# Kernel tuning notes

Hardware: AMD Instinct MI355X
Metric: run time of the kernel (lower is better)

## Reference

```python
import jax, jax.numpy as jnp
import numpy as np

B, C, H, Wd = 16, 256, 64, 64
D_MODEL = 256


def setup_inputs() -> dict:
    key = jax.random.key(0)
    kx, kw = jax.random.split(key)
    x = jax.random.normal(kx, (B, C, H, Wd), dtype=jnp.float32)
    # 1x1 conv weight [out_c=1+2*d_model, in_c], scaled like kaiming-ish init
    W = jax.random.normal(kw, (1 + 2 * D_MODEL, C), dtype=jnp.float32) / np.sqrt(C)
    return {"x": x, "W": W}


def reference(x, W):
    b, c, h, w = x.shape
    d = (W.shape[0] - 1) // 2
    n = h * w
    xf = x.reshape(b, c, n)                      # [b, c, N]
    qkv = jnp.einsum('oc,bcn->bon', W, xf)       # 1x1 conv == channel GEMM
    q = qkv[:, :1]                               # [b, 1, N]
    k = qkv[:, 1:1 + d]                          # [b, d, N]
    v = qkv[:, 1 + d:]                           # [b, d, N]
    scores = jax.nn.softmax(q, axis=-1)          # softmax over tokens
    ctx = jnp.sum(k * scores, axis=-1, keepdims=True)  # [b, d, 1]
    out = jax.nn.relu(v) * ctx                   # gated ReLU(v)
    return out.reshape(b, d, h, w)
```

## Files before the change

kernel.cpp:

```cpp
#include <hip/hip_runtime.h>
#include <cstdint>
#include <cstddef>

#define NB 16
#define NC 256
#define NN 4096
#define ND 256

typedef unsigned short u16;
typedef unsigned int u32;

typedef __attribute__((ext_vector_type(8))) short short8;
typedef __attribute__((ext_vector_type(4))) float f32x4;

__device__ __forceinline__ u16 f2bf(float f) {
  union { float f; u32 u; } v; v.f = f;
  u32 r = v.u + 0x7FFFu + ((v.u >> 16) & 1u);
  return (u16)(r >> 16);
}
__device__ __forceinline__ float bf2f(u16 h) {
  union { u32 u; float f; } v; v.u = ((u32)h) << 16; return v.f;
}

__global__ __launch_bounds__(256) void k_zero(float* __restrict__ q,
                                              float* __restrict__ xs) {
  const int i = blockIdx.x * 256 + threadIdx.x;
  if (i < NB * NN) q[i] = 0.f;
  else xs[i - NB * NN] = 0.f;
}

__global__ __launch_bounds__(256) void k_cast_transpose_q(const float* __restrict__ x,
                                                          const float* __restrict__ W,
                                                          u16* __restrict__ xbT,
                                                          float* __restrict__ q) {
  __shared__ __align__(16) u16 tile[64 * 68];
  __shared__ float qred[16 * 64];
  const int t = threadIdx.x;
  const int b = blockIdx.z, c0 = blockIdx.y * 64, n0 = blockIdx.x * 64;
  const float* xb = x + (size_t)(b * NC + c0) * NN + n0;
  const int nl = (t & 15) * 4;
  float qacc[4] = {0.f, 0.f, 0.f, 0.f};
#pragma unroll
  for (int i = 0; i < 4; ++i) {
    int cl = (t >> 4) + i * 16;
    float4 v = *(const float4*)(xb + (size_t)cl * NN + nl);
    const float wq = W[c0 + cl];
    qacc[0] += wq * v.x; qacc[1] += wq * v.y;
    qacc[2] += wq * v.z; qacc[3] += wq * v.w;
    tile[(nl + 0) * 68 + cl] = f2bf(v.x);
    tile[(nl + 1) * 68 + cl] = f2bf(v.y);
    tile[(nl + 2) * 68 + cl] = f2bf(v.z);
    tile[(nl + 3) * 68 + cl] = f2bf(v.w);
  }
#pragma unroll
  for (int j = 0; j < 4; ++j) qred[(t >> 4) * 64 + nl + j] = qacc[j];
  __syncthreads();
  u16* ob = xbT + (size_t)(b * NN + n0) * NC + c0;
#pragma unroll
  for (int i = 0; i < 4; ++i) {
    int e = t + i * 256;
    int rn = e >> 4;
    int rc = (e & 15) * 4;
    ushort4 pv = *(const ushort4*)&tile[rn * 68 + rc];
    *(ushort4*)(ob + (size_t)rn * NC + rc) = pv;
  }
  if (t < 64) {
    float s = 0.f;
#pragma unroll
    for (int k = 0; k < 16; ++k) s += qred[k * 64 + t];
    atomicAdd(&q[b * NN + n0 + t], s);
  }
}

__global__ __launch_bounds__(256) void k_softmax(const float* __restrict__ q,
                                                 float* __restrict__ s) {
  __shared__ float red[256];
  const int b = blockIdx.x, t = threadIdx.x;
  const float* qb = q + b * NN;
  float v[16];
  float m = -3.4e38f;
#pragma unroll
  for (int i = 0; i < 16; ++i) { v[i] = qb[t + i * 256]; m = fmaxf(m, v[i]); }
  red[t] = m;
  __syncthreads();
  for (int off = 128; off > 0; off >>= 1) {
    if (t < off) red[t] = fmaxf(red[t], red[t + off]);
    __syncthreads();
  }
  const float M = red[0];
  __syncthreads();
  float sum = 0.f;
#pragma unroll
  for (int i = 0; i < 16; ++i) { v[i] = __expf(v[i] - M); sum += v[i]; }
  red[t] = sum;
  __syncthreads();
  for (int off = 128; off > 0; off >>= 1) {
    if (t < off) red[t] += red[t + off];
    __syncthreads();
  }
  const float inv = 1.f / red[0];
  float* sb = s + b * NN;
#pragma unroll
  for (int i = 0; i < 16; ++i) sb[t + i * 256] = v[i] * inv;
}

__global__ __launch_bounds__(256) void k_xs(const u16* __restrict__ xbT,
                                            const float* __restrict__ s,
                                            float* __restrict__ xs) {
  const int t = threadIdx.x;
  const int b = blockIdx.y, n0 = blockIdx.x * 128;
  const u16* xp = xbT + ((size_t)(b * NN + n0)) * NC + t;
  const float* sp = s + b * NN + n0;
  float acc = 0.f;
#pragma unroll 8
  for (int j = 0; j < 128; ++j) {
    acc += bf2f(xp[(size_t)j * NC]) * sp[j];
  }
  atomicAdd(&xs[b * NC + t], acc);
}

__global__ __launch_bounds__(256) void k_ctx(const float* __restrict__ W,
                                             const float* __restrict__ xs,
                                             float* __restrict__ ctx) {
  __shared__ float sx[NC];
  const int b = blockIdx.x, d = threadIdx.x;
  sx[d] = xs[b * NC + d];
  __syncthreads();
  const float* wk = W + (size_t)(1 + d) * NC;
  float acc = 0.f;
#pragma unroll 4
  for (int c = 0; c < NC; ++c) acc += wk[c] * sx[c];
  ctx[b * NC + d] = acc;
}

__global__ __launch_bounds__(256) void k_castwv(const float* __restrict__ W,
                                                u16* __restrict__ wvb) {
  const int i = (blockIdx.x * 256 + threadIdx.x) * 4;
  const float4 v = *(const float4*)(W + (size_t)(1 + ND) * NC + i);
  ushort4 o;
  o.x = f2bf(v.x); o.y = f2bf(v.y); o.z = f2bf(v.z); o.w = f2bf(v.w);
  *(ushort4*)(wvb + i) = o;
}

#define BM 128
#define BN 128
#define BK 64

__global__ __launch_bounds__(256) void k_gemm(const u16* __restrict__ xbT,
                                              const u16* __restrict__ wvb,
                                              const float* __restrict__ ctx,
                                              float* __restrict__ out) {
  __shared__ __align__(16) u16 As[BM * BK];
  __shared__ __align__(16) u16 Bs[BN * BK];
  const int t = threadIdx.x;
  const int b = blockIdx.z;
  const int d0 = blockIdx.y * BM;
  const int n0 = blockIdx.x * BN;
  const int lane = t & 63, w = t >> 6;
  const int wd = (w & 1) * 64, wn = (w >> 1) * 64;
  const int quad = lane >> 4, l15 = lane & 15;

  f32x4 acc[4][4];
#pragma unroll
  for (int mi = 0; mi < 4; ++mi)
#pragma unroll
    for (int ni = 0; ni < 4; ++ni)
      acc[mi][ni] = (f32x4){0.f, 0.f, 0.f, 0.f};

  const int rstg = t >> 3;
  const int l8 = (((t & 7) ^ (rstg & 7))) * 8;
  const u16* gA = wvb + (size_t)(d0 + rstg) * NC + l8;
  const u16* gB = xbT + (size_t)(b * NN + n0 + rstg) * NC + l8;
  const int ldst = 8 * t;

  const int pq0 = ((0 * 4 + quad) ^ (l15 & 7)) * 8;
  const int pq1 = ((1 * 4 + quad) ^ (l15 & 7)) * 8;

  for (int kk = 0; kk < NC; kk += BK) {
    __syncthreads();
#pragma unroll
    for (int i = 0; i < 4; ++i) {
      __builtin_amdgcn_global_load_lds(
          (const __attribute__((address_space(1))) u32*)(gA + kk + (size_t)(32 * i) * NC),
          (__attribute__((address_space(3))) u32*)(As + 2048 * i + ldst), 16, 0, 0);
      __builtin_amdgcn_global_load_lds(
          (const __attribute__((address_space(1))) u32*)(gB + kk + (size_t)(32 * i) * NC),
          (__attribute__((address_space(3))) u32*)(Bs + 2048 * i + ldst), 16, 0, 0);
    }
    __syncthreads();

#pragma unroll
    for (int kq = 0; kq < 2; ++kq) {
      const int pq = kq ? pq1 : pq0;
      short8 af[4], bfr[4];
#pragma unroll
      for (int mi = 0; mi < 4; ++mi)
        af[mi] = *(const short8*)&As[(wd + mi * 16 + l15) * BK + pq];
#pragma unroll
      for (int ni = 0; ni < 4; ++ni)
        bfr[ni] = *(const short8*)&Bs[(wn + ni * 16 + l15) * BK + pq];
#pragma unroll
      for (int mi = 0; mi < 4; ++mi)
#pragma unroll
        for (int ni = 0; ni < 4; ++ni)
          acc[mi][ni] = __builtin_amdgcn_mfma_f32_16x16x32_bf16(af[mi], bfr[ni],
                                                                acc[mi][ni], 0, 0, 0);
    }
  }

#pragma unroll
  for (int mi = 0; mi < 4; ++mi) {
#pragma unroll
    for (int r = 0; r < 4; ++r) {
      const int d = d0 + wd + mi * 16 + quad * 4 + r;
      const float cx = ctx[b * NC + d];
      float* op = out + (size_t)(b * NC + d) * NN + n0 + wn + l15;
#pragma unroll
      for (int ni = 0; ni < 4; ++ni) {
        float v = acc[mi][ni][r];
        op[ni * 16] = fmaxf(v, 0.f) * cx;
      }
    }
  }
}

extern "C" void kernel_launch(void* const* d_in, const int* in_sizes, int n_in,
                              void* d_out, int out_size, void* d_ws, size_t ws_size,
                              hipStream_t stream) {
  const float* x = (const float*)d_in[0];
  const float* W = (const float*)d_in[1];
  float* out = (float*)d_out;

  char* ws = (char*)d_ws;
  u16* xbT   = (u16*)ws;
  float* q   = (float*)(ws + 33554432);
  float* s   = (float*)(ws + 33554432 + 262144);
  float* xs  = (float*)(ws + 33554432 + 524288);
  float* ctx = (float*)(ws + 33554432 + 540672);
  u16* wvb   = (u16*)(ws + 33554432 + 557056);

  k_zero<<<272, 256, 0, stream>>>(q, xs);
  k_cast_transpose_q<<<dim3(64, 4, 16), 256, 0, stream>>>(x, W, xbT, q);
  k_softmax<<<16, 256, 0, stream>>>(q, s);
  k_xs<<<dim3(32, 16), 256, 0, stream>>>(xbT, s, xs);
  k_ctx<<<16, 256, 0, stream>>>(W, xs, ctx);
  k_castwv<<<64, 256, 0, stream>>>(W, wvb);
  k_gemm<<<dim3(32, 2, 16), 256, 0, stream>>>(xbT, wvb, ctx, out);
}
```

Measured before the change: 155.0 us.

## Fuse q projection, online softmax partials and cast into one pass, enlarge GEMM tile

Replaces the zero, cast-transpose, softmax, xs-reduction, ctx and weight-cast kernels with two kernels. The first computes q, per-tile softmax max/sum and weighted x partials over a 64-token tile covering all channels, and also writes the transposed bf16 x. The second combines the partials flash-style and computes ctx while casting Wv. This removes the atomics and the extra re-read of xbT. The GEMM moves to 256x128 tiles with 512 threads covering all of d per block, which halves grid size and increases LDS use.

```diff
diff --git a/kernel.cpp b/kernel.cpp
--- a/kernel.cpp
+++ b/kernel.cpp
@@ -22,142 +22,120 @@
   union { u32 u; float f; } v; v.u = ((u32)h) << 16; return v.f;
 }
 
-__global__ __launch_bounds__(256) void k_zero(float* __restrict__ q,
-                                              float* __restrict__ xs) {
-  const int i = blockIdx.x * 256 + threadIdx.x;
-  if (i < NB * NN) q[i] = 0.f;
-  else xs[i - NB * NN] = 0.f;
-}
-
-__global__ __launch_bounds__(256) void k_cast_transpose_q(const float* __restrict__ x,
-                                                          const float* __restrict__ W,
-                                                          u16* __restrict__ xbT,
-                                                          float* __restrict__ q) {
-  __shared__ __align__(16) u16 tile[64 * 68];
+__global__ __launch_bounds__(256) void k_fuse1(const float* __restrict__ x,
+                                               const float* __restrict__ W,
+                                               u16* __restrict__ xbT,
+                                               float* __restrict__ pm,
+                                               float* __restrict__ pl,
+                                               float* __restrict__ pacc) {
+  __shared__ __align__(16) u16 tile[64 * 264];
   __shared__ float qred[16 * 64];
+  __shared__ float qv[64];
+  __shared__ float pv[64];
   const int t = threadIdx.x;
-  const int b = blockIdx.z, c0 = blockIdx.y * 64, n0 = blockIdx.x * 64;
-  const float* xb = x + (size_t)(b * NC + c0) * NN + n0;
+  const int b = blockIdx.y, n0 = blockIdx.x * 64;
+  const float* xb = x + (size_t)b * NC * NN + n0;
   const int nl = (t & 15) * 4;
-  float qacc[4] = {0.f, 0.f, 0.f, 0.f};
-#pragma unroll
-  for (int i = 0; i < 4; ++i) {
-    int cl = (t >> 4) + i * 16;
-    float4 v = *(const float4*)(xb + (size_t)cl * NN + nl);
-    const float wq = W[c0 + cl];
-    qacc[0] += wq * v.x; qacc[1] += wq * v.y;
-    qacc[2] += wq * v.z; qacc[3] += wq * v.w;
-    tile[(nl + 0) * 68 + cl] = f2bf(v.x);
-    tile[(nl + 1) * 68 + cl] = f2bf(v.y);
-    tile[(nl + 2) * 68 + cl] = f2bf(v.z);
-    tile[(nl + 3) * 68 + cl] = f2bf(v.w);
-  }
-#pragma unroll
-  for (int j = 0; j < 4; ++j) qred[(t >> 4) * 64 + nl + j] = qacc[j];
-  __syncthreads();
-  u16* ob = xbT + (size_t)(b * NN + n0) * NC + c0;
-#pragma unroll
-  for (int i = 0; i < 4; ++i) {
-    int e = t + i * 256;
-    int rn = e >> 4;
-    int rc = (e & 15) * 4;
-    ushort4 pv = *(const ushort4*)&tile[rn * 68 + rc];
-    *(ushort4*)(ob + (size_t)rn * NC + rc) = pv;
-  }
+  const int cg = t >> 4;
+  float q0 = 0.f, q1 = 0.f, q2 = 0.f, q3 = 0.f;
+#pragma unroll
+  for (int i = 0; i < 16; ++i) {
+    const int c = cg + i * 16;
+    float4 v = *(const float4*)(xb + (size_t)c * NN + nl);
+    const float wq = W[c];
+    q0 += wq * v.x; q1 += wq * v.y; q2 += wq * v.z; q3 += wq * v.w;
+    tile[(nl + 0) * 264 + c] = f2bf(v.x);
+    tile[(nl + 1) * 264 + c] = f2bf(v.y);
+    tile[(nl + 2) * 264 + c] = f2bf(v.z);
+    tile[(nl + 3) * 264 + c] = f2bf(v.w);
+  }
+  qred[cg * 64 + nl + 0] = q0;
+  qred[cg * 64 + nl + 1] = q1;
+  qred[cg * 64 + nl + 2] = q2;
+  qred[cg * 64 + nl + 3] = q3;
+  __syncthreads();
   if (t < 64) {
     float s = 0.f;
 #pragma unroll
     for (int k = 0; k < 16; ++k) s += qred[k * 64 + t];
-    atomicAdd(&q[b * NN + n0 + t], s);
-  }
-}
-
-__global__ __launch_bounds__(256) void k_softmax(const float* __restrict__ q,
-                                                 float* __restrict__ s) {
-  __shared__ float red[256];
-  const int b = blockIdx.x, t = threadIdx.x;
-  const float* qb = q + b * NN;
-  float v[16];
-  float m = -3.4e38f;
-#pragma unroll
-  for (int i = 0; i < 16; ++i) { v[i] = qb[t + i * 256]; m = fmaxf(m, v[i]); }
-  red[t] = m;
-  __syncthreads();
-  for (int off = 128; off > 0; off >>= 1) {
-    if (t < off) red[t] = fmaxf(red[t], red[t + off]);
-    __syncthreads();
-  }
-  const float M = red[0];
-  __syncthreads();
-  float sum = 0.f;
-#pragma unroll
-  for (int i = 0; i < 16; ++i) { v[i] = __expf(v[i] - M); sum += v[i]; }
-  red[t] = sum;
-  __syncthreads();
-  for (int off = 128; off > 0; off >>= 1) {
-    if (t < off) red[t] += red[t + off];
-    __syncthreads();
-  }
-  const float inv = 1.f / red[0];
-  float* sb = s + b * NN;
-#pragma unroll
-  for (int i = 0; i < 16; ++i) sb[t + i * 256] = v[i] * inv;
-}
-
-__global__ __launch_bounds__(256) void k_xs(const u16* __restrict__ xbT,
-                                            const float* __restrict__ s,
-                                            float* __restrict__ xs) {
-  const int t = threadIdx.x;
-  const int b = blockIdx.y, n0 = blockIdx.x * 128;
-  const u16* xp = xbT + ((size_t)(b * NN + n0)) * NC + t;
-  const float* sp = s + b * NN + n0;
+    qv[t] = s;
+  }
+  __syncthreads();
+  float m = qv[0];
+#pragma unroll 16
+  for (int n = 1; n < 64; ++n) m = fmaxf(m, qv[n]);
+  if (t < 64) pv[t] = __expf(qv[t] - m);
+  __syncthreads();
   float acc = 0.f;
 #pragma unroll 8
-  for (int j = 0; j < 128; ++j) {
-    acc += bf2f(xp[(size_t)j * NC]) * sp[j];
-  }
-  atomicAdd(&xs[b * NC + t], acc);
-}
-
-__global__ __launch_bounds__(256) void k_ctx(const float* __restrict__ W,
-                                             const float* __restrict__ xs,
-                                             float* __restrict__ ctx) {
+  for (int n = 0; n < 64; ++n) acc += bf2f(tile[n * 264 + t]) * pv[n];
+  pacc[((size_t)b * 64 + blockIdx.x) * NC + t] = acc;
+  if (t == 0) {
+    float l = 0.f;
+    for (int n = 0; n < 64; ++n) l += pv[n];
+    pm[b * 64 + blockIdx.x] = m;
+    pl[b * 64 + blockIdx.x] = l;
+  }
+  u16* ob = xbT + (size_t)(b * NN + n0) * NC;
+#pragma unroll
+  for (int i = 0; i < 8; ++i) {
+    const int e = t + i * 256;
+    const int rn = e >> 5;
+    const int rc = (e & 31) * 8;
+    *(short8*)(ob + (size_t)rn * NC + rc) = *(const short8*)&tile[rn * 264 + rc];
+  }
+}
+
+__global__ __launch_bounds__(256) void k_combine(const float* __restrict__ W,
+                                                 const float* __restrict__ pm,
+                                                 const float* __restrict__ pl,
+                                                 const float* __restrict__ pacc,
+                                                 float* __restrict__ ctx,
+                                                 u16* __restrict__ wvb) {
+  __shared__ float sm[64], sl[64], sw[64];
   __shared__ float sx[NC];
-  const int b = blockIdx.x, d = threadIdx.x;
-  sx[d] = xs[b * NC + d];
-  __syncthreads();
-  const float* wk = W + (size_t)(1 + d) * NC;
-  float acc = 0.f;
+  const int b = blockIdx.x, t = threadIdx.x;
+  if (t < 64) { sm[t] = pm[b * 64 + t]; sl[t] = pl[b * 64 + t]; }
+  __syncthreads();
+  float M = -3.4e38f;
+#pragma unroll 16
+  for (int i = 0; i < 64; ++i) M = fmaxf(M, sm[i]);
+  if (t < 64) sw[t] = __expf(sm[t] - M);
+  __syncthreads();
+  float L = 0.f;
+#pragma unroll 16
+  for (int i = 0; i < 64; ++i) L += sw[i] * sl[i];
+  float xsc = 0.f;
+#pragma unroll 8
+  for (int i = 0; i < 64; ++i) xsc += sw[i] * pacc[((size_t)b * 64 + i) * NC + t];
+  sx[t] = xsc / L;
+  __syncthreads();
+  const float* wk = W + (size_t)(1 + t) * NC;
+  float a = 0.f;
 #pragma unroll 4
-  for (int c = 0; c < NC; ++c) acc += wk[c] * sx[c];
-  ctx[b * NC + d] = acc;
-}
-
-__global__ __launch_bounds__(256) void k_castwv(const float* __restrict__ W,
-                                                u16* __restrict__ wvb) {
-  const int i = (blockIdx.x * 256 + threadIdx.x) * 4;
-  const float4 v = *(const float4*)(W + (size_t)(1 + ND) * NC + i);
-  ushort4 o;
-  o.x = f2bf(v.x); o.y = f2bf(v.y); o.z = f2bf(v.z); o.w = f2bf(v.w);
-  *(ushort4*)(wvb + i) = o;
-}
-
-#define BM 128
+  for (int c = 0; c < NC; ++c) a += wk[c] * sx[c];
+  ctx[b * NC + t] = a;
+  const float* wv = W + (size_t)(1 + ND) * NC + (size_t)b * 16 * NC;
+  u16* wo = wvb + (size_t)b * 16 * NC;
+#pragma unroll
+  for (int i = 0; i < 16; ++i) wo[i * NC + t] = f2bf(wv[i * NC + t]);
+}
+
+#define BM 256
 #define BN 128
 #define BK 64
 
-__global__ __launch_bounds__(256) void k_gemm(const u16* __restrict__ xbT,
+__global__ __launch_bounds__(512) void k_gemm(const u16* __restrict__ xbT,
                                               const u16* __restrict__ wvb,
                                               const float* __restrict__ ctx,
                                               float* __restrict__ out) {
   __shared__ __align__(16) u16 As[BM * BK];
   __shared__ __align__(16) u16 Bs[BN * BK];
   const int t = threadIdx.x;
-  const int b = blockIdx.z;
-  const int d0 = blockIdx.y * BM;
+  const int b = blockIdx.y;
   const int n0 = blockIdx.x * BN;
   const int lane = t & 63, w = t >> 6;
-  const int wd = (w & 1) * 64, wn = (w >> 1) * 64;
+  const int wd = (w >> 1) * 64, wn = (w & 1) * 64;
   const int quad = lane >> 4, l15 = lane & 15;
 
   f32x4 acc[4][4];
@@ -168,8 +146,8 @@
       acc[mi][ni] = (f32x4){0.f, 0.f, 0.f, 0.f};
 
   const int rstg = t >> 3;
-  const int l8 = (((t & 7) ^ (rstg & 7))) * 8;
-  const u16* gA = wvb + (size_t)(d0 + rstg) * NC + l8;
+  const int l8 = ((t & 7) ^ (rstg & 7)) * 8;
+  const u16* gA = wvb + (size_t)rstg * NC + l8;
   const u16* gB = xbT + (size_t)(b * NN + n0 + rstg) * NC + l8;
   const int ldst = 8 * t;
 
@@ -179,14 +157,15 @@
   for (int kk = 0; kk < NC; kk += BK) {
     __syncthreads();
 #pragma unroll
-    for (int i = 0; i < 4; ++i) {
+    for (int i = 0; i < 4; ++i)
       __builtin_amdgcn_global_load_lds(
-          (const __attribute__((address_space(1))) u32*)(gA + kk + (size_t)(32 * i) * NC),
-          (__attribute__((address_space(3))) u32*)(As + 2048 * i + ldst), 16, 0, 0);
+          (const __attribute__((address_space(1))) u32*)(gA + kk + (size_t)(64 * i) * NC),
+          (__attribute__((address_space(3))) u32*)(As + 4096 * i + ldst), 16, 0, 0);
+#pragma unroll
+    for (int i = 0; i < 2; ++i)
       __builtin_amdgcn_global_load_lds(
-          (const __attribute__((address_space(1))) u32*)(gB + kk + (size_t)(32 * i) * NC),
-          (__attribute__((address_space(3))) u32*)(Bs + 2048 * i + ldst), 16, 0, 0);
-    }
+          (const __attribute__((address_space(1))) u32*)(gB + kk + (size_t)(64 * i) * NC),
+          (__attribute__((address_space(3))) u32*)(Bs + 4096 * i + ldst), 16, 0, 0);
     __syncthreads();
 
 #pragma unroll
@@ -212,7 +191,7 @@
   for (int mi = 0; mi < 4; ++mi) {
 #pragma unroll
     for (int r = 0; r < 4; ++r) {
-      const int d = d0 + wd + mi * 16 + quad * 4 + r;
+      const int d = wd + mi * 16 + quad * 4 + r;
       const float cx = ctx[b * NC + d];
       float* op = out + (size_t)(b * NC + d) * NN + n0 + wn + l15;
 #pragma unroll
@@ -232,18 +211,14 @@
   float* out = (float*)d_out;
 
   char* ws = (char*)d_ws;
-  u16* xbT   = (u16*)ws;
-  float* q   = (float*)(ws + 33554432);
-  float* s   = (float*)(ws + 33554432 + 262144);
-  float* xs  = (float*)(ws + 33554432 + 524288);
-  float* ctx = (float*)(ws + 33554432 + 540672);
-  u16* wvb   = (u16*)(ws + 33554432 + 557056);
-
-  k_zero<<<272, 256, 0, stream>>>(q, xs);
-  k_cast_transpose_q<<<dim3(64, 4, 16), 256, 0, stream>>>(x, W, xbT, q);
-  k_softmax<<<16, 256, 0, stream>>>(q, s);
-  k_xs<<<dim3(32, 16), 256, 0, stream>>>(xbT, s, xs);
-  k_ctx<<<16, 256, 0, stream>>>(W, xs, ctx);
-  k_castwv<<<64, 256, 0, stream>>>(W, wvb);
-  k_gemm<<<dim3(32, 2, 16), 256, 0, stream>>>(xbT, wvb, ctx, out);
-}
+  u16* xbT    = (u16*)ws;
+  float* pacc = (float*)(ws + 33554432);
+  float* pm   = (float*)(ws + 34603008);
+  float* pl   = (float*)(ws + 34607104);
+  float* ctx  = (float*)(ws + 34611200);
+  u16* wvb    = (u16*)(ws + 34627584);
+
+  k_fuse1<<<dim3(64, 16), 256, 0, stream>>>(x, W, xbT, pm, pl, pacc);
+  k_combine<<<16, 256, 0, stream>>>(W, pm, pl, pacc, ctx, wvb);
+  k_gemm<<<dim3(32, 16), 512, 0, stream>>>(xbT, wvb, ctx, out);
+}
```

New measurement: 149.6 us. 1.04x faster.
